# Kernel tuning notes

Hardware: AMD Instinct MI355X
Metric: run time of the kernel (lower is better)

The kernel has to match this reference:

```python
import jax, jax.numpy as jnp
import numpy as np
import math

D_MODEL = 512
NUM_HEADS = 8
HEAD_DIM = D_MODEL // NUM_HEADS
B, L = 2, 2048
LN_EPS = 1e-5
DEN_EPS = 1e-5


def setup_inputs() -> dict:
    key = jax.random.key(0)
    ks = jax.random.split(key, 6)
    s = 1.0 / math.sqrt(D_MODEL)
    return {
        "x": jax.random.normal(ks[0], (B, L, D_MODEL), dtype=jnp.float32),
        "Wqkv": jax.random.normal(ks[1], (D_MODEL, 3 * D_MODEL), dtype=jnp.float32) * s,
        "bqkv": jnp.zeros((3 * D_MODEL,), dtype=jnp.float32),
        "Wout": jax.random.normal(ks[2], (D_MODEL, D_MODEL), dtype=jnp.float32) * s,
        "bout": jnp.zeros((D_MODEL,), dtype=jnp.float32),
        "ln_gamma": jnp.ones((D_MODEL,), dtype=jnp.float32),
        "ln_beta": jnp.zeros((D_MODEL,), dtype=jnp.float32),
        "decay_logits": jnp.full((NUM_HEADS,), 5.0, dtype=jnp.float32),
    }


def reference(x, Wqkv, bqkv, Wout, bout, ln_gamma, ln_beta, decay_logits):
    Bv, Lv, D = x.shape
    H = decay_logits.shape[0]
    E = D // H

    qkv = x @ Wqkv + bqkv                                   # [B,L,3D]
    q, k, v = jnp.split(qkv, 3, axis=-1)
    q = q.reshape(Bv, Lv, H, E)
    k = k.reshape(Bv, Lv, H, E)
    v = v.reshape(Bv, Lv, H, E)

    # ELU feature map + 1 -> positive features; scale q by 1/sqrt(E)
    q = (jax.nn.elu(q) + 1.0) / jnp.sqrt(jnp.asarray(E, x.dtype))
    k = jax.nn.elu(k) + 1.0

    lambdas = jax.nn.sigmoid(decay_logits).reshape(1, 1, H, 1)   # [1,1,H,1]
    t = jnp.arange(Lv, dtype=x.dtype).reshape(1, Lv, 1, 1)       # [1,L,1,1]
    decay_k = jnp.power(lambdas, -t)   # lambda^{-t}
    decay_q = jnp.power(lambdas, t)    # lambda^{t}

    k_dec = k * decay_k                                          # [B,L,H,E]
    kv = jnp.einsum('blhe,blhf->blhef', k_dec, v)                # [B,L,H,E,E]
    memory = jnp.cumsum(kv, axis=1)                              # prefix-sum scan over L
    k_sum = jnp.cumsum(k_dec, axis=1)                            # [B,L,H,E]

    q_dec = q * decay_q
    num = jnp.einsum('blhe,blhef->blhf', q_dec, memory)          # [B,L,H,E]
    den = jnp.einsum('blhe,blhe->blh', q_dec, k_sum)[..., None] + DEN_EPS
    out = (num / den).reshape(Bv, Lv, D)

    out = out @ Wout + bout

    # LayerNorm (eval mode; dropout is identity)
    mu = jnp.mean(out, axis=-1, keepdims=True)
    var = jnp.var(out, axis=-1, keepdims=True)
    out = (out - mu) / jnp.sqrt(var + LN_EPS) * ln_gamma + ln_beta
    return out
```

## Files before the change

kernel.cpp:

```cpp
#include <hip/hip_runtime.h>
#include <math.h>

#define B_ 2
#define L_ 2048
#define D_ 512
#define H_ 8
#define E_ 64
#define CHUNK 32
#define NCH 64
#define DEN_EPS_ 1e-5f
#define LN_EPS_ 1e-5f

typedef __bf16 bf16x8 __attribute__((ext_vector_type(8)));
typedef __bf16 bf16x4 __attribute__((ext_vector_type(4)));
typedef float  f32x4  __attribute__((ext_vector_type(4)));

__device__ __forceinline__ float sigm(float x) { return 1.f / (1.f + expf(-x)); }
__device__ __forceinline__ float elu1(float x) { return x > 0.f ? x + 1.f : expf(x); }

__device__ __forceinline__ void async_cp16(const void* g, void* l) {
    __builtin_amdgcn_global_load_lds(
        (const __attribute__((address_space(1))) void*)g,
        (__attribute__((address_space(3))) void*)l, 16, 0, 0);
}

#define SWZ4(row, q) ((((q) ^ ((row) & 3)) * 8))

__global__ __launch_bounds__(256) void k_prep_w(
    const float* __restrict__ W1, __bf16* __restrict__ D1,
    const float* __restrict__ W2, __bf16* __restrict__ D2)
{
    const int t = threadIdx.x;
    const int bx = blockIdx.x;
    const float* src; __bf16* dst; int N, xt;
    if (bx < 24) { src = W1; dst = D1; N = 1536; xt = bx; }
    else         { src = W2; dst = D2; N = 512;  xt = bx - 24; }
    const int K = 512;

    __shared__ __bf16 tile[64][68];
    const int kb = blockIdx.y * 64, nb = xt * 64;
    const int rr = t >> 4, cc4 = (t & 15) * 4;
#pragma unroll
    for (int p = 0; p < 4; p++) {
        int k = rr + p * 16;
        float4 v = *(const float4*)&src[(size_t)(kb + k) * N + nb + cc4];
        tile[k][cc4 + 0] = (__bf16)v.x;
        tile[k][cc4 + 1] = (__bf16)v.y;
        tile[k][cc4 + 2] = (__bf16)v.z;
        tile[k][cc4 + 3] = (__bf16)v.w;
    }
    __syncthreads();
#pragma unroll
    for (int p = 0; p < 4; p++) {
        int n = rr + p * 16;
        bf16x4 o;
        o[0] = tile[cc4 + 0][n];
        o[1] = tile[cc4 + 1][n];
        o[2] = tile[cc4 + 2][n];
        o[3] = tile[cc4 + 3][n];
        *(bf16x4*)&dst[(size_t)(nb + n) * K + kb + cc4] = o;
    }
}

__global__ __launch_bounds__(256) void k_mfma_qkv_g(
    const float* __restrict__ X, const __bf16* __restrict__ Bt,
    const float* __restrict__ bias, const float* __restrict__ dl,
    __bf16* __restrict__ Qb, __bf16* __restrict__ Kb, __bf16* __restrict__ Vb,
    __bf16* __restrict__ Gt, float* __restrict__ gn)
{
    __shared__ __bf16 lds[28672];
    const int t = threadIdx.x;
    const int w = t >> 6, lane = t & 63;
    const int wm = w >> 1, wn = w & 1;
    const int ll = lane & 15, quad = lane >> 4;
    const int m0 = blockIdx.y * 64, n0 = blockIdx.x * 128;
    const int h0 = n0 >> 6;

    f32x4 acc[3][2][4] = {};
    const int sr = t >> 2;
    const int c4 = t & 3;
    const int skz = ((c4 ^ (sr & 3)) * 8);

    float4 pa0, pa1;
    auto fetchA = [&](int k0) {
        const float* ap = X + (size_t)(m0 + sr) * D_ + k0 + skz;
        pa0 = *(const float4*)ap;
        pa1 = *(const float4*)(ap + 4);
    };
    auto issueB = [&](int k0, int buf) {
        const int bb = buf * 14336 + 2048;
#pragma unroll
        for (int s = 0; s < 3; s++)
#pragma unroll
            for (int half = 0; half < 2; half++)
                async_cp16(&Bt[(size_t)(s * 512 + n0 + half * 64 + sr) * D_ + k0 + skz],
                           &lds[bb + s * 4096 + (half * 64 + w * 16) * 32]);
    };
    auto writeA = [&](int buf) {
        bf16x8 o;
        o[0] = (__bf16)pa0.x; o[1] = (__bf16)pa0.y;
        o[2] = (__bf16)pa0.z; o[3] = (__bf16)pa0.w;
        o[4] = (__bf16)pa1.x; o[5] = (__bf16)pa1.y;
        o[6] = (__bf16)pa1.z; o[7] = (__bf16)pa1.w;
        *(bf16x8*)&lds[buf * 14336 + sr * 32 + c4 * 8] = o;
    };

    fetchA(0);
    issueB(0, 0);
    writeA(0);
    __syncthreads();

    for (int k0 = 0; k0 < D_; k0 += 32) {
        const int buf = (k0 >> 5) & 1, nbuf = buf ^ 1;
        const int nk = k0 + 32;
        if (nk < D_) { fetchA(nk); issueB(nk, nbuf); }
        const int ao = buf * 14336, bo = ao + 2048;
        bf16x8 afr[2];
#pragma unroll
        for (int im = 0; im < 2; im++) {
            int ra = wm * 32 + im * 16 + ll;
            afr[im] = *(const bf16x8*)&lds[ao + ra * 32 + SWZ4(ra, quad)];
        }
#pragma unroll
        for (int s = 0; s < 3; s++) {
            bf16x8 bfr[4];
#pragma unroll
            for (int in = 0; in < 4; in++) {
                int rb = wn * 64 + in * 16 + ll;
                bfr[in] = *(const bf16x8*)&lds[bo + s * 4096 + rb * 32 + SWZ4(rb, quad)];
            }
#pragma unroll
            for (int im = 0; im < 2; im++)
#pragma unroll
                for (int in = 0; in < 4; in++)
                    acc[s][im][in] = __builtin_amdgcn_mfma_f32_16x16x32_bf16(
                        afr[im], bfr[in], acc[s][im][in], 0, 0, 0);
        }
        if (nk < D_) writeA(nbuf);
        __syncthreads();
    }

    const int h = h0 + wn;
    const float lam = sigm(dl[h]);
    const float l2  = log2f(lam);
    __bf16* Kwt = &lds[w * 4096];
    __bf16* Vtw = &lds[w * 4096 + 2048];

    float wk8[2][4];
#pragma unroll
    for (int im = 0; im < 2; im++)
#pragma unroll
        for (int r = 0; r < 4; r++) {
            int i = (im * 16 + quad * 4 + r) & 31;
            wk8[im][r] = exp2f(l2 * (float)(CHUNK - 1 - i));
        }

#pragma unroll
    for (int im = 0; im < 2; im++) {
#pragma unroll
        for (int in = 0; in < 4; in++) {
            int nc = wn * 64 + in * 16 + ll;
            int e  = nc & 63;
            float bq = bias[n0 + nc];
            float bk = bias[512 + n0 + nc];
            float bv = bias[1024 + n0 + nc];
#pragma unroll
            for (int r = 0; r < 4; r++) {
                int mr = wm * 32 + im * 16 + quad * 4 + r;
                int m = m0 + mr, bb2 = m >> 11, l = m & 2047;
                size_t off = ((size_t)((bb2 * H_ + h) * L_ + l)) * E_ + e;
                float vq = elu1(acc[0][im][in][r] + bq) * 0.125f;
                float vk = elu1(acc[1][im][in][r] + bk);
                float vv = acc[2][im][in][r] + bv;
                Qb[off] = (__bf16)vq;
                Kb[off] = (__bf16)vk;
                Vb[off] = (__bf16)vv;
                int i = mr & 31;
                int col = ((i >> 3) ^ (e & 3)) * 8 + (i & 7);
                Kwt[e * 32 + col] = (__bf16)(vk * wk8[im][r]);
                Vtw[e * 32 + col] = (__bf16)vv;
            }
        }
    }

    const int bb2 = m0 >> 11;
    const int bh = bb2 * H_ + h;
    const int nchunk = ((m0 & 2047) >> 5) + wm;

    {
        float ga = 0.f;
#pragma unroll
        for (int ci = 0; ci < 4; ci++) {
            int colb = ((ci ^ (lane & 3)) * 8);
#pragma unroll
            for (int j = 0; j < 8; j++) ga += (float)Kwt[lane * 32 + colb + j];
        }
        gn[((size_t)bh * NCH + nchunk) * E_ + lane] = ga;
    }

    f32x4 gac[4][4] = {};
#pragma unroll
    for (int a = 0; a < 4; a++) {
        int raf = a * 16 + ll;
        bf16x8 av = *(const bf16x8*)&Vtw[raf * 32 + SWZ4(raf, quad)];
#pragma unroll
        for (int b2 = 0; b2 < 4; b2++) {
            int rbe = b2 * 16 + ll;
            bf16x8 kv = *(const bf16x8*)&Kwt[rbe * 32 + SWZ4(rbe, quad)];
            gac[a][b2] = __builtin_amdgcn_mfma_f32_16x16x32_bf16(av, kv, gac[a][b2], 0, 0, 0);
        }
    }
    size_t gbase = ((size_t)bh * NCH + nchunk) * 4096;
#pragma unroll
    for (int a = 0; a < 4; a++)
#pragma unroll
        for (int b2 = 0; b2 < 4; b2++)
#pragma unroll
            for (int r = 0; r < 4; r++) {
                int f = a * 16 + quad * 4 + r;
                int e = b2 * 16 + ll;
                Gt[gbase + (size_t)f * 64 + e] = (__bf16)gac[a][b2][r];
            }
}

__global__ __launch_bounds__(64) void k_scan_par(
    const __bf16* __restrict__ Gt, const float* __restrict__ gn,
    const float* __restrict__ dl,
    __bf16* __restrict__ Sb, float* __restrict__ zl)
{
    const int lane = threadIdx.x;
    const int bh = blockIdx.x >> 6;
    const int j  = blockIdx.x & 63;
    const float lam = sigm(dl[bh & 7]);
    const float dC  = exp2f(32.f * log2f(lam));

    const size_t base = ((size_t)bh * NCH) * 4096 + (size_t)j * 64 + lane;

    __bf16 g[NCH];
#pragma unroll
    for (int n = 0; n < NCH; n++) g[n] = Gt[base + (size_t)n * 4096];

    float s = 0.f;
#pragma unroll
    for (int n = 0; n < NCH; n++) {
        Sb[base + (size_t)n * 4096] = (__bf16)(lam * s);
        s = fmaf(dC, s, (float)g[n]);
    }

    float gv = gn[((size_t)bh * NCH + lane) * E_ + j];
    float wf = dC;
#pragma unroll
    for (int k = 1; k < 64; k <<= 1) {
        float up = __shfl_up(gv, k);
        if (lane >= k) gv = fmaf(wf, up, gv);
        wf = wf * wf;
    }
    float zex = __shfl_up(gv, 1);
    if (lane == 0) zex = 0.f;
    zl[((size_t)bh * NCH + lane) * E_ + j] = lam * zex;
}

__global__ __launch_bounds__(256) void k_attn(
    const __bf16* __restrict__ Qb, const __bf16* __restrict__ Kb,
    const __bf16* __restrict__ Vb,
    const __bf16* __restrict__ Sb, const float* __restrict__ zl,
    const float* __restrict__ dl, __bf16* __restrict__ Out)
{
    __shared__ __bf16 Qw[32][64];
    __shared__ __bf16 Kw[32][64];
    __shared__ __bf16 Vt[64][40];
    __shared__ __bf16 A1[32][40];
    __shared__ float  den[32];
    __shared__ float  zz[64];

    const int t  = threadIdx.x;
    const int bx = blockIdx.x;
    const int n = bx & 63, h = (bx >> 6) & 7, bb = bx >> 9;
    const int bh = bb * H_ + h;
    const float lam = sigm(dl[h]);
    const float l2  = log2f(lam);

    const int w = t >> 6, lane = t & 63;
    const int ll = lane & 15, quad = lane >> 4;
    const int fw = w * 16;
    const size_t sbase = ((size_t)bh * NCH + n) * 4096;

    bf16x8 bS0 = *(const bf16x8*)&Sb[sbase + (size_t)(fw + ll) * 64 + quad * 8];
    bf16x8 bS1 = *(const bf16x8*)&Sb[sbase + (size_t)(fw + ll) * 64 + 32 + quad * 8];

    {
        int i = t >> 3, e0c = t & 7;
        size_t src = ((size_t)bh * L_ + n * CHUNK + i) * E_ + e0c * 8;
        float wq = exp2f(l2 * (float)i);
        float wk = exp2f(-l2 * (float)i);
        bf16x8 q8 = *(const bf16x8*)&Qb[src];
        bf16x8 k8 = *(const bf16x8*)&Kb[src];
        bf16x8 v8 = *(const bf16x8*)&Vb[src];
        bf16x8 qo, ko;
        int e0 = e0c * 8;
#pragma unroll
        for (int q = 0; q < 8; q++) {
            qo[q] = (__bf16)((float)q8[q] * wq);
            ko[q] = (__bf16)((float)k8[q] * wk);
            Vt[e0 + q][i] = v8[q];
        }
        int cs = (e0c ^ (i & 7)) * 8;
        *(bf16x8*)&Qw[i][cs] = qo;
        *(bf16x8*)&Kw[i][cs] = ko;
        if (t < 64) zz[t] = zl[((size_t)bh * NCH + n) * E_ + t];
    }
    __syncthreads();

    {
        const int wm = w >> 1, wn = w & 1;
        int ra = wm * 16 + ll, rb = wn * 16 + ll;
        f32x4 accA = {};
#pragma unroll
        for (int ks = 0; ks < 2; ks++) {
            bf16x8 a = *(const bf16x8*)&Qw[ra][((ks * 4 + quad) ^ (ra & 7)) * 8];
            bf16x8 b = *(const bf16x8*)&Kw[rb][((ks * 4 + quad) ^ (rb & 7)) * 8];
            accA = __builtin_amdgcn_mfma_f32_16x16x32_bf16(a, b, accA, 0, 0, 0);
        }
        int j = wn * 16 + ll;
#pragma unroll
        for (int r = 0; r < 4; r++) {
            int i = wm * 16 + quad * 4 + r;
            A1[i][j] = (__bf16)(j <= i ? accA[r] : 0.f);
        }
    }
    __syncthreads();

    if (t < 32) {
        float rs = 0.f;
#pragma unroll
        for (int k8 = 0; k8 < 4; k8++) {
            bf16x8 aa = *(const bf16x8*)&A1[t][k8 * 8];
#pragma unroll
            for (int q = 0; q < 8; q++) rs += (float)aa[q];
        }
        float qz = 0.f;
#pragma unroll
        for (int e8 = 0; e8 < 8; e8++) {
            bf16x8 qq = *(const bf16x8*)&Qw[t][(e8 ^ (t & 7)) * 8];
#pragma unroll
            for (int q = 0; q < 8; q++) qz += (float)qq[q] * zz[e8 * 8 + q];
        }
        den[t] = rs + qz + DEN_EPS_;
    }

    f32x4 acc1[2] = {}, acc2[2] = {};
    {
        bf16x8 bV = *(const bf16x8*)&Vt[fw + ll][quad * 8];
#pragma unroll
        for (int im = 0; im < 2; im++) {
            bf16x8 aA = *(const bf16x8*)&A1[im * 16 + ll][quad * 8];
            acc1[im] = __builtin_amdgcn_mfma_f32_16x16x32_bf16(aA, bV, acc1[im], 0, 0, 0);
        }
#pragma unroll
        for (int im = 0; im < 2; im++) {
            int ra = im * 16 + ll;
            bf16x8 aQ0 = *(const bf16x8*)&Qw[ra][((quad) ^ (ra & 7)) * 8];
            bf16x8 aQ1 = *(const bf16x8*)&Qw[ra][((4 + quad) ^ (ra & 7)) * 8];
            acc2[im] = __builtin_amdgcn_mfma_f32_16x16x32_bf16(aQ0, bS0, acc2[im], 0, 0, 0);
            acc2[im] = __builtin_amdgcn_mfma_f32_16x16x32_bf16(aQ1, bS1, acc2[im], 0, 0, 0);
        }
    }
    __syncthreads();

#pragma unroll
    for (int im = 0; im < 2; im++)
#pragma unroll
        for (int r = 0; r < 4; r++) {
            int i = im * 16 + quad * 4 + r;
            float o = (acc1[im][r] + acc2[im][r]) / den[i];
            Out[((size_t)bb * L_ + n * CHUNK + i) * D_ + h * E_ + fw + ll] = (__bf16)o;
        }
}

__global__ __launch_bounds__(256) void k_mfma_out_ln(
    const __bf16* __restrict__ Ab, const __bf16* __restrict__ Bt,
    const float* __restrict__ bias, const float* __restrict__ gam,
    const float* __restrict__ bet, float* __restrict__ Y)
{
    __shared__ __bf16 lds[33792];
    __shared__ float gaml[512], betl[512], bl[512];
    __shared__ float redS[4][16], redQ[4][16];
    __shared__ float mv[16][2];

    const int t = threadIdx.x;
    const int w = t >> 6, lane = t & 63;
    const int ll = lane & 15, quad = lane >> 4;
    const int m0 = blockIdx.x * 16;

    {
        float2 g = *(const float2*)&gam[t * 2];
        float2 b2 = *(const float2*)&bet[t * 2];
        float2 bo = *(const float2*)&bias[t * 2];
        gaml[t * 2] = g.x;  gaml[t * 2 + 1] = g.y;
        betl[t * 2] = b2.x; betl[t * 2 + 1] = b2.y;
        bl[t * 2]   = bo.x; bl[t * 2 + 1]   = bo.y;
    }

    f32x4 acc[8] = {};
    const int sr  = t >> 2;
    const int skz = (((t & 3) ^ (sr & 3)) * 8);

    auto issue = [&](int k0, int buf) {
        if (t < 64)
            async_cp16(&Ab[(size_t)(m0 + sr) * D_ + k0 + skz], &lds[buf * 512]);
#pragma unroll
        for (int p = 0; p < 8; p++)
            async_cp16(&Bt[(size_t)(p * 64 + sr) * D_ + k0 + skz],
                       &lds[1024 + buf * 16384 + (p * 64 + w * 16) * 32]);
    };

    issue(0, 0);
    __syncthreads();

    for (int k0 = 0; k0 < D_; k0 += 32) {
        const int buf = (k0 >> 5) & 1, nbuf = buf ^ 1;
        const int nk = k0 + 32;
        if (nk < D_) issue(nk, nbuf);
        const int ao = buf * 512, bo = 1024 + buf * 16384;
        bf16x8 a = *(const bf16x8*)&lds[ao + ll * 32 + SWZ4(ll, quad)];
#pragma unroll
        for (int in = 0; in < 8; in++) {
            int rb = w * 128 + in * 16 + ll;
            bf16x8 b = *(const bf16x8*)&lds[bo + rb * 32 + SWZ4(rb, quad)];
            acc[in] = __builtin_amdgcn_mfma_f32_16x16x32_bf16(a, b, acc[in], 0, 0, 0);
        }
        __syncthreads();
    }

    float vals[8][4];
    float ps[4] = {}, pq[4] = {};
#pragma unroll
    for (int in = 0; in < 8; in++) {
        int col = w * 128 + in * 16 + ll;
        float bv = bl[col];
#pragma unroll
        for (int r = 0; r < 4; r++) {
            float v = acc[in][r] + bv;
            vals[in][r] = v;
            ps[r] += v;
            pq[r] += v * v;
        }
    }
#pragma unroll
    for (int r = 0; r < 4; r++) {
        float s = ps[r], q = pq[r];
        s += __shfl_xor(s, 1); q += __shfl_xor(q, 1);
        s += __shfl_xor(s, 2); q += __shfl_xor(q, 2);
        s += __shfl_xor(s, 4); q += __shfl_xor(q, 4);
        s += __shfl_xor(s, 8); q += __shfl_xor(q, 8);
        if (ll == 0) {
            int row = quad * 4 + r;
            redS[w][row] = s;
            redQ[w][row] = q;
        }
    }
    __syncthreads();
    if (t < 16) {
        float S = redS[0][t] + redS[1][t] + redS[2][t] + redS[3][t];
        float Q = redQ[0][t] + redQ[1][t] + redQ[2][t] + redQ[3][t];
        float mu  = S * (1.f / 512.f);
        float var = Q * (1.f / 512.f) - mu * mu;
        mv[t][0] = mu;
        mv[t][1] = rsqrtf(var + LN_EPS_);
    }
    __syncthreads();
#pragma unroll
    for (int r = 0; r < 4; r++) {
        int row = quad * 4 + r;
        float mu = mv[row][0], rs = mv[row][1];
#pragma unroll
        for (int in = 0; in < 8; in++) {
            int col = w * 128 + in * 16 + ll;
            Y[(size_t)(m0 + row) * D_ + col] =
                (vals[in][r] - mu) * rs * gaml[col] + betl[col];
        }
    }
}

extern "C" void kernel_launch(void* const* d_in, const int* in_sizes, int n_in,
                              void* d_out, int out_size, void* d_ws, size_t ws_size,
                              hipStream_t stream)
{
    const float* x    = (const float*)d_in[0];
    const float* Wqkv = (const float*)d_in[1];
    const float* bqkv = (const float*)d_in[2];
    const float* Wout = (const float*)d_in[3];
    const float* bout = (const float*)d_in[4];
    const float* gam  = (const float*)d_in[5];
    const float* bet  = (const float*)d_in[6];
    const float* dl   = (const float*)d_in[7];
    float* out = (float*)d_out;

    const size_t NBHLE = (size_t)B_ * H_ * L_ * E_;
    const size_t NG    = (size_t)B_ * H_ * NCH * E_ * E_;
    const size_t Ng    = (size_t)B_ * H_ * NCH * E_;

    char* p = (char*)d_ws;
    __bf16* Gt  = (__bf16*)p;    p += NG * 2;
    __bf16* Sb  = (__bf16*)p;    p += NG * 2;
    float*  gn  = (float*)p;     p += Ng * 4;
    float*  zl  = (float*)p;     p += Ng * 4;
    __bf16* Qb  = (__bf16*)p;    p += NBHLE * 2;
    __bf16* Kb  = (__bf16*)p;    p += NBHLE * 2;
    __bf16* Vb  = (__bf16*)p;    p += NBHLE * 2;
    __bf16* WqkvT = (__bf16*)p;  p += (size_t)1536 * 512 * 2;
    __bf16* WoutT = (__bf16*)p;  p += (size_t)512 * 512 * 2;
    __bf16* Ao    = (__bf16*)p;  p += NBHLE * 2;

    dim3 blk(256);
    k_prep_w      <<<dim3(32, 8), blk, 0, stream>>>(Wqkv, WqkvT, Wout, WoutT);
    k_mfma_qkv_g  <<<dim3(4, 64), blk, 0, stream>>>(x, WqkvT, bqkv, dl,
                                                    Qb, Kb, Vb, Gt, gn);
    k_scan_par    <<<dim3(1024),  dim3(64), 0, stream>>>(Gt, gn, dl, Sb, zl);
    k_attn        <<<dim3(1024),  blk, 0, stream>>>(Qb, Kb, Vb, Sb, zl, dl, Ao);
    k_mfma_out_ln <<<dim3(256),   blk, 0, stream>>>(Ao, WoutT, bout, gam, bet, out);
}
```

Baseline: 128.6 us.

## Fuse all stages into one persistent kernel with grid-wide atomic barriers

Replaces the five separate kernel launches with a single persistent kernel of 256 blocks. The stages (weight transpose, QKV GEMM, scan, chunked attention, output GEMM with LayerNorm) are separated by software grid barriers built on atomic counters, and each stage reuses one shared-memory buffer. This is meant to remove launch overhead and inter-kernel gaps. In exchange, stages that used 1024 blocks now loop inside 256 blocks, the output GEMM loses its double buffering, and correctness depends on all 256 blocks being co-resident.

```diff
diff --git a/kernel.cpp b/kernel.cpp
--- a/kernel.cpp
+++ b/kernel.cpp
@@ -10,6 +10,7 @@
 #define NCH 64
 #define DEN_EPS_ 1e-5f
 #define LN_EPS_ 1e-5f
+#define NBLK 256
 
 typedef __bf16 bf16x8 __attribute__((ext_vector_type(8)));
 typedef __bf16 bf16x4 __attribute__((ext_vector_type(4)));
@@ -26,458 +27,460 @@
 
 #define SWZ4(row, q) ((((q) ^ ((row) & 3)) * 8))
 
-__global__ __launch_bounds__(256) void k_prep_w(
-    const float* __restrict__ W1, __bf16* __restrict__ D1,
-    const float* __restrict__ W2, __bf16* __restrict__ D2)
-{
-    const int t = threadIdx.x;
-    const int bx = blockIdx.x;
-    const float* src; __bf16* dst; int N, xt;
-    if (bx < 24) { src = W1; dst = D1; N = 1536; xt = bx; }
-    else         { src = W2; dst = D2; N = 512;  xt = bx - 24; }
-    const int K = 512;
-
-    __shared__ __bf16 tile[64][68];
-    const int kb = blockIdx.y * 64, nb = xt * 64;
-    const int rr = t >> 4, cc4 = (t & 15) * 4;
-#pragma unroll
-    for (int p = 0; p < 4; p++) {
-        int k = rr + p * 16;
-        float4 v = *(const float4*)&src[(size_t)(kb + k) * N + nb + cc4];
-        tile[k][cc4 + 0] = (__bf16)v.x;
-        tile[k][cc4 + 1] = (__bf16)v.y;
-        tile[k][cc4 + 2] = (__bf16)v.z;
-        tile[k][cc4 + 3] = (__bf16)v.w;
+__device__ __forceinline__ void gbar(unsigned int* bar, int idx) {
+    __syncthreads();
+    if (threadIdx.x == 0) {
+        __threadfence();
+        atomicAdd(&bar[idx], 1u);
+        while (__hip_atomic_load(&bar[idx], __ATOMIC_RELAXED,
+                                 __HIP_MEMORY_SCOPE_AGENT) < (unsigned)NBLK)
+            __builtin_amdgcn_s_sleep(8);
+        __threadfence();
     }
     __syncthreads();
-#pragma unroll
-    for (int p = 0; p < 4; p++) {
-        int n = rr + p * 16;
-        bf16x4 o;
-        o[0] = tile[cc4 + 0][n];
-        o[1] = tile[cc4 + 1][n];
-        o[2] = tile[cc4 + 2][n];
-        o[3] = tile[cc4 + 3][n];
-        *(bf16x4*)&dst[(size_t)(nb + n) * K + kb + cc4] = o;
-    }
 }
 
-__global__ __launch_bounds__(256) void k_mfma_qkv_g(
-    const float* __restrict__ X, const __bf16* __restrict__ Bt,
-    const float* __restrict__ bias, const float* __restrict__ dl,
+struct AttnS {
+    __bf16 Qw[32][64];
+    __bf16 Kw[32][64];
+    __bf16 Vt[64][40];
+    __bf16 A1[32][40];
+    float  den[32];
+    float  zz[64];
+};
+struct OutS {
+    __bf16 lds[16896];
+    float  gaml[512], betl[512], bl[512];
+    float  redS[4][16], redQ[4][16];
+    float  mv[16][2];
+};
+
+__global__ __launch_bounds__(256) void k_mega(
+    const float* __restrict__ X,  const float* __restrict__ W1,
+    const float* __restrict__ W2, const float* __restrict__ bqkv,
+    const float* __restrict__ bout, const float* __restrict__ gam,
+    const float* __restrict__ bet,  const float* __restrict__ dl,
+    __bf16* __restrict__ WqkvT, __bf16* __restrict__ WoutT,
     __bf16* __restrict__ Qb, __bf16* __restrict__ Kb, __bf16* __restrict__ Vb,
-    __bf16* __restrict__ Gt, float* __restrict__ gn)
+    __bf16* __restrict__ Gt, float* __restrict__ gn,
+    __bf16* __restrict__ Sb, float* __restrict__ zl,
+    __bf16* __restrict__ Ao, float* __restrict__ out,
+    unsigned int* bar)
 {
-    __shared__ __bf16 lds[28672];
-    const int t = threadIdx.x;
-    const int w = t >> 6, lane = t & 63;
-    const int wm = w >> 1, wn = w & 1;
-    const int ll = lane & 15, quad = lane >> 4;
-    const int m0 = blockIdx.y * 64, n0 = blockIdx.x * 128;
-    const int h0 = n0 >> 6;
-
-    f32x4 acc[3][2][4] = {};
-    const int sr = t >> 2;
-    const int c4 = t & 3;
-    const int skz = ((c4 ^ (sr & 3)) * 8);
-
-    float4 pa0, pa1;
-    auto fetchA = [&](int k0) {
-        const float* ap = X + (size_t)(m0 + sr) * D_ + k0 + skz;
-        pa0 = *(const float4*)ap;
-        pa1 = *(const float4*)(ap + 4);
-    };
-    auto issueB = [&](int k0, int buf) {
-        const int bb = buf * 14336 + 2048;
-#pragma unroll
-        for (int s = 0; s < 3; s++)
-#pragma unroll
-            for (int half = 0; half < 2; half++)
-                async_cp16(&Bt[(size_t)(s * 512 + n0 + half * 64 + sr) * D_ + k0 + skz],
-                           &lds[bb + s * 4096 + (half * 64 + w * 16) * 32]);
-    };
-    auto writeA = [&](int buf) {
-        bf16x8 o;
-        o[0] = (__bf16)pa0.x; o[1] = (__bf16)pa0.y;
-        o[2] = (__bf16)pa0.z; o[3] = (__bf16)pa0.w;
-        o[4] = (__bf16)pa1.x; o[5] = (__bf16)pa1.y;
-        o[6] = (__bf16)pa1.z; o[7] = (__bf16)pa1.w;
-        *(bf16x8*)&lds[buf * 14336 + sr * 32 + c4 * 8] = o;
-    };
-
-    fetchA(0);
-    issueB(0, 0);
-    writeA(0);
-    __syncthreads();
-
-    for (int k0 = 0; k0 < D_; k0 += 32) {
-        const int buf = (k0 >> 5) & 1, nbuf = buf ^ 1;
-        const int nk = k0 + 32;
-        if (nk < D_) { fetchA(nk); issueB(nk, nbuf); }
-        const int ao = buf * 14336, bo = ao + 2048;
-        bf16x8 afr[2];
-#pragma unroll
-        for (int im = 0; im < 2; im++) {
-            int ra = wm * 32 + im * 16 + ll;
-            afr[im] = *(const bf16x8*)&lds[ao + ra * 32 + SWZ4(ra, quad)];
-        }
-#pragma unroll
-        for (int s = 0; s < 3; s++) {
-            bf16x8 bfr[4];
-#pragma unroll
-            for (int in = 0; in < 4; in++) {
-                int rb = wn * 64 + in * 16 + ll;
-                bfr[in] = *(const bf16x8*)&lds[bo + s * 4096 + rb * 32 + SWZ4(rb, quad)];
-            }
-#pragma unroll
-            for (int im = 0; im < 2; im++)
-#pragma unroll
-                for (int in = 0; in < 4; in++)
-                    acc[s][im][in] = __builtin_amdgcn_mfma_f32_16x16x32_bf16(
-                        afr[im], bfr[in], acc[s][im][in], 0, 0, 0);
-        }
-        if (nk < D_) writeA(nbuf);
-        __syncthreads();
-    }
-
-    const int h = h0 + wn;
-    const float lam = sigm(dl[h]);
-    const float l2  = log2f(lam);
-    __bf16* Kwt = &lds[w * 4096];
-    __bf16* Vtw = &lds[w * 4096 + 2048];
-
-    float wk8[2][4];
-#pragma unroll
-    for (int im = 0; im < 2; im++)
-#pragma unroll
-        for (int r = 0; r < 4; r++) {
-            int i = (im * 16 + quad * 4 + r) & 31;
-            wk8[im][r] = exp2f(l2 * (float)(CHUNK - 1 - i));
-        }
-
-#pragma unroll
-    for (int im = 0; im < 2; im++) {
-#pragma unroll
-        for (int in = 0; in < 4; in++) {
-            int nc = wn * 64 + in * 16 + ll;
-            int e  = nc & 63;
-            float bq = bias[n0 + nc];
-            float bk = bias[512 + n0 + nc];
-            float bv = bias[1024 + n0 + nc];
-#pragma unroll
-            for (int r = 0; r < 4; r++) {
-                int mr = wm * 32 + im * 16 + quad * 4 + r;
-                int m = m0 + mr, bb2 = m >> 11, l = m & 2047;
-                size_t off = ((size_t)((bb2 * H_ + h) * L_ + l)) * E_ + e;
-                float vq = elu1(acc[0][im][in][r] + bq) * 0.125f;
-                float vk = elu1(acc[1][im][in][r] + bk);
-                float vv = acc[2][im][in][r] + bv;
-                Qb[off] = (__bf16)vq;
-                Kb[off] = (__bf16)vk;
-                Vb[off] = (__bf16)vv;
-                int i = mr & 31;
-                int col = ((i >> 3) ^ (e & 3)) * 8 + (i & 7);
-                Kwt[e * 32 + col] = (__bf16)(vk * wk8[im][r]);
-                Vtw[e * 32 + col] = (__bf16)vv;
-            }
-        }
-    }
-
-    const int bb2 = m0 >> 11;
-    const int bh = bb2 * H_ + h;
-    const int nchunk = ((m0 & 2047) >> 5) + wm;
-
-    {
-        float ga = 0.f;
-#pragma unroll
-        for (int ci = 0; ci < 4; ci++) {
-            int colb = ((ci ^ (lane & 3)) * 8);
-#pragma unroll
-            for (int j = 0; j < 8; j++) ga += (float)Kwt[lane * 32 + colb + j];
-        }
-        gn[((size_t)bh * NCH + nchunk) * E_ + lane] = ga;
-    }
-
-    f32x4 gac[4][4] = {};
-#pragma unroll
-    for (int a = 0; a < 4; a++) {
-        int raf = a * 16 + ll;
-        bf16x8 av = *(const bf16x8*)&Vtw[raf * 32 + SWZ4(raf, quad)];
-#pragma unroll
-        for (int b2 = 0; b2 < 4; b2++) {
-            int rbe = b2 * 16 + ll;
-            bf16x8 kv = *(const bf16x8*)&Kwt[rbe * 32 + SWZ4(rbe, quad)];
-            gac[a][b2] = __builtin_amdgcn_mfma_f32_16x16x32_bf16(av, kv, gac[a][b2], 0, 0, 0);
-        }
-    }
-    size_t gbase = ((size_t)bh * NCH + nchunk) * 4096;
-#pragma unroll
-    for (int a = 0; a < 4; a++)
-#pragma unroll
-        for (int b2 = 0; b2 < 4; b2++)
-#pragma unroll
-            for (int r = 0; r < 4; r++) {
-                int f = a * 16 + quad * 4 + r;
-                int e = b2 * 16 + ll;
-                Gt[gbase + (size_t)f * 64 + e] = (__bf16)gac[a][b2][r];
-            }
-}
-
-__global__ __launch_bounds__(64) void k_scan_par(
-    const __bf16* __restrict__ Gt, const float* __restrict__ gn,
-    const float* __restrict__ dl,
-    __bf16* __restrict__ Sb, float* __restrict__ zl)
-{
-    const int lane = threadIdx.x;
-    const int bh = blockIdx.x >> 6;
-    const int j  = blockIdx.x & 63;
-    const float lam = sigm(dl[bh & 7]);
-    const float dC  = exp2f(32.f * log2f(lam));
-
-    const size_t base = ((size_t)bh * NCH) * 4096 + (size_t)j * 64 + lane;
-
-    __bf16 g[NCH];
-#pragma unroll
-    for (int n = 0; n < NCH; n++) g[n] = Gt[base + (size_t)n * 4096];
-
-    float s = 0.f;
-#pragma unroll
-    for (int n = 0; n < NCH; n++) {
-        Sb[base + (size_t)n * 4096] = (__bf16)(lam * s);
-        s = fmaf(dC, s, (float)g[n]);
-    }
-
-    float gv = gn[((size_t)bh * NCH + lane) * E_ + j];
-    float wf = dC;
-#pragma unroll
-    for (int k = 1; k < 64; k <<= 1) {
-        float up = __shfl_up(gv, k);
-        if (lane >= k) gv = fmaf(wf, up, gv);
-        wf = wf * wf;
-    }
-    float zex = __shfl_up(gv, 1);
-    if (lane == 0) zex = 0.f;
-    zl[((size_t)bh * NCH + lane) * E_ + j] = lam * zex;
-}
-
-__global__ __launch_bounds__(256) void k_attn(
-    const __bf16* __restrict__ Qb, const __bf16* __restrict__ Kb,
-    const __bf16* __restrict__ Vb,
-    const __bf16* __restrict__ Sb, const float* __restrict__ zl,
-    const float* __restrict__ dl, __bf16* __restrict__ Out)
-{
-    __shared__ __bf16 Qw[32][64];
-    __shared__ __bf16 Kw[32][64];
-    __shared__ __bf16 Vt[64][40];
-    __shared__ __bf16 A1[32][40];
-    __shared__ float  den[32];
-    __shared__ float  zz[64];
-
+    __shared__ __align__(16) char smem[57344];
     const int t  = threadIdx.x;
-    const int bx = blockIdx.x;
-    const int n = bx & 63, h = (bx >> 6) & 7, bb = bx >> 9;
-    const int bh = bb * H_ + h;
-    const float lam = sigm(dl[h]);
-    const float l2  = log2f(lam);
-
+    const int vb = blockIdx.x;
     const int w = t >> 6, lane = t & 63;
     const int ll = lane & 15, quad = lane >> 4;
-    const int fw = w * 16;
-    const size_t sbase = ((size_t)bh * NCH + n) * 4096;
-
-    bf16x8 bS0 = *(const bf16x8*)&Sb[sbase + (size_t)(fw + ll) * 64 + quad * 8];
-    bf16x8 bS1 = *(const bf16x8*)&Sb[sbase + (size_t)(fw + ll) * 64 + 32 + quad * 8];
 
     {
-        int i = t >> 3, e0c = t & 7;
-        size_t src = ((size_t)bh * L_ + n * CHUNK + i) * E_ + e0c * 8;
-        float wq = exp2f(l2 * (float)i);
-        float wk = exp2f(-l2 * (float)i);
-        bf16x8 q8 = *(const bf16x8*)&Qb[src];
-        bf16x8 k8 = *(const bf16x8*)&Kb[src];
-        bf16x8 v8 = *(const bf16x8*)&Vb[src];
-        bf16x8 qo, ko;
-        int e0 = e0c * 8;
-#pragma unroll
-        for (int q = 0; q < 8; q++) {
-            qo[q] = (__bf16)((float)q8[q] * wq);
-            ko[q] = (__bf16)((float)k8[q] * wk);
-            Vt[e0 + q][i] = v8[q];
-        }
-        int cs = (e0c ^ (i & 7)) * 8;
-        *(bf16x8*)&Qw[i][cs] = qo;
-        *(bf16x8*)&Kw[i][cs] = ko;
-        if (t < 64) zz[t] = zl[((size_t)bh * NCH + n) * E_ + t];
+        __bf16 (*tile)[68] = (__bf16(*)[68])smem;
+        const int xt_ = vb & 31, ky = vb >> 5;
+        const float* src; __bf16* dst; int N, xt;
+        if (xt_ < 24) { src = W1; dst = WqkvT; N = 1536; xt = xt_; }
+        else          { src = W2; dst = WoutT; N = 512;  xt = xt_ - 24; }
+        const int K = 512;
+        const int kb = ky * 64, nb = xt * 64;
+        const int rr = t >> 4, cc4 = (t & 15) * 4;
+#pragma unroll
+        for (int p = 0; p < 4; p++) {
+            int k = rr + p * 16;
+            float4 v = *(const float4*)&src[(size_t)(kb + k) * N + nb + cc4];
+            tile[k][cc4 + 0] = (__bf16)v.x;
+            tile[k][cc4 + 1] = (__bf16)v.y;
+            tile[k][cc4 + 2] = (__bf16)v.z;
+            tile[k][cc4 + 3] = (__bf16)v.w;
+        }
+        __syncthreads();
+#pragma unroll
+        for (int p = 0; p < 4; p++) {
+            int n = rr + p * 16;
+            bf16x4 o;
+            o[0] = tile[cc4 + 0][n];
+            o[1] = tile[cc4 + 1][n];
+            o[2] = tile[cc4 + 2][n];
+            o[3] = tile[cc4 + 3][n];
+            *(bf16x4*)&dst[(size_t)(nb + n) * K + kb + cc4] = o;
+        }
     }
-    __syncthreads();
+    gbar(bar, 0);
 
     {
+        __bf16* lds = (__bf16*)smem;
         const int wm = w >> 1, wn = w & 1;
-        int ra = wm * 16 + ll, rb = wn * 16 + ll;
-        f32x4 accA = {};
-#pragma unroll
-        for (int ks = 0; ks < 2; ks++) {
-            bf16x8 a = *(const bf16x8*)&Qw[ra][((ks * 4 + quad) ^ (ra & 7)) * 8];
-            bf16x8 b = *(const bf16x8*)&Kw[rb][((ks * 4 + quad) ^ (rb & 7)) * 8];
-            accA = __builtin_amdgcn_mfma_f32_16x16x32_bf16(a, b, accA, 0, 0, 0);
-        }
-        int j = wn * 16 + ll;
-#pragma unroll
-        for (int r = 0; r < 4; r++) {
-            int i = wm * 16 + quad * 4 + r;
-            A1[i][j] = (__bf16)(j <= i ? accA[r] : 0.f);
-        }
+        const int m0 = (vb >> 2) * 64, n0 = (vb & 3) * 128;
+        const int h0 = n0 >> 6;
+
+        f32x4 acc[3][2][4] = {};
+        const int sr = t >> 2;
+        const int c4 = t & 3;
+        const int skz = ((c4 ^ (sr & 3)) * 8);
+
+        float4 pa0, pa1;
+        auto fetchA = [&](int k0) {
+            const float* ap = X + (size_t)(m0 + sr) * D_ + k0 + skz;
+            pa0 = *(const float4*)ap;
+            pa1 = *(const float4*)(ap + 4);
+        };
+        auto issueB = [&](int k0, int buf) {
+            const int bb = buf * 14336 + 2048;
+#pragma unroll
+            for (int s = 0; s < 3; s++)
+#pragma unroll
+                for (int half = 0; half < 2; half++)
+                    async_cp16(&WqkvT[(size_t)(s * 512 + n0 + half * 64 + sr) * D_ + k0 + skz],
+                               &lds[bb + s * 4096 + (half * 64 + w * 16) * 32]);
+        };
+        auto writeA = [&](int buf) {
+            bf16x8 o;
+            o[0] = (__bf16)pa0.x; o[1] = (__bf16)pa0.y;
+            o[2] = (__bf16)pa0.z; o[3] = (__bf16)pa0.w;
+            o[4] = (__bf16)pa1.x; o[5] = (__bf16)pa1.y;
+            o[6] = (__bf16)pa1.z; o[7] = (__bf16)pa1.w;
+            *(bf16x8*)&lds[buf * 14336 + sr * 32 + c4 * 8] = o;
+        };
+
+        fetchA(0);
+        issueB(0, 0);
+        writeA(0);
+        __syncthreads();
+
+        for (int k0 = 0; k0 < D_; k0 += 32) {
+            const int buf = (k0 >> 5) & 1, nbuf = buf ^ 1;
+            const int nk = k0 + 32;
+            if (nk < D_) { fetchA(nk); issueB(nk, nbuf); }
+            const int ao = buf * 14336, bo = ao + 2048;
+            bf16x8 afr[2];
+#pragma unroll
+            for (int im = 0; im < 2; im++) {
+                int ra = wm * 32 + im * 16 + ll;
+                afr[im] = *(const bf16x8*)&lds[ao + ra * 32 + SWZ4(ra, quad)];
+            }
+#pragma unroll
+            for (int s = 0; s < 3; s++) {
+                bf16x8 bfr[4];
+#pragma unroll
+                for (int in = 0; in < 4; in++) {
+                    int rb = wn * 64 + in * 16 + ll;
+                    bfr[in] = *(const bf16x8*)&lds[bo + s * 4096 + rb * 32 + SWZ4(rb, quad)];
+                }
+#pragma unroll
+                for (int im = 0; im < 2; im++)
+#pragma unroll
+                    for (int in = 0; in < 4; in++)
+                        acc[s][im][in] = __builtin_amdgcn_mfma_f32_16x16x32_bf16(
+                            afr[im], bfr[in], acc[s][im][in], 0, 0, 0);
+            }
+            if (nk < D_) writeA(nbuf);
+            __syncthreads();
+        }
+
+        const int h = h0 + wn;
+        const float lam = sigm(dl[h]);
+        const float l2  = log2f(lam);
+        __bf16* Kwt = &lds[w * 4096];
+        __bf16* Vtw = &lds[w * 4096 + 2048];
+
+        float wk8[2][4];
+#pragma unroll
+        for (int im = 0; im < 2; im++)
+#pragma unroll
+            for (int r = 0; r < 4; r++) {
+                int i = (im * 16 + quad * 4 + r) & 31;
+                wk8[im][r] = exp2f(l2 * (float)(CHUNK - 1 - i));
+            }
+
+#pragma unroll
+        for (int im = 0; im < 2; im++) {
+#pragma unroll
+            for (int in = 0; in < 4; in++) {
+                int nc = wn * 64 + in * 16 + ll;
+                int e  = nc & 63;
+                float bq = bqkv[n0 + nc];
+                float bk = bqkv[512 + n0 + nc];
+                float bv = bqkv[1024 + n0 + nc];
+#pragma unroll
+                for (int r = 0; r < 4; r++) {
+                    int mr = wm * 32 + im * 16 + quad * 4 + r;
+                    int m = m0 + mr, bb2 = m >> 11, l = m & 2047;
+                    size_t off = ((size_t)((bb2 * H_ + h) * L_ + l)) * E_ + e;
+                    float vq = elu1(acc[0][im][in][r] + bq) * 0.125f;
+                    float vk = elu1(acc[1][im][in][r] + bk);
+                    float vv = acc[2][im][in][r] + bv;
+                    Qb[off] = (__bf16)vq;
+                    Kb[off] = (__bf16)vk;
+                    Vb[off] = (__bf16)vv;
+                    int i = mr & 31;
+                    int col = ((i >> 3) ^ (e & 3)) * 8 + (i & 7);
+                    Kwt[e * 32 + col] = (__bf16)(vk * wk8[im][r]);
+                    Vtw[e * 32 + col] = (__bf16)vv;
+                }
+            }
+        }
+
+        const int bb2 = m0 >> 11;
+        const int bh = bb2 * H_ + h;
+        const int nchunk = ((m0 & 2047) >> 5) + wm;
+
+        {
+            float ga = 0.f;
+#pragma unroll
+            for (int ci = 0; ci < 4; ci++) {
+                int colb = ((ci ^ (lane & 3)) * 8);
+#pragma unroll
+                for (int j = 0; j < 8; j++) ga += (float)Kwt[lane * 32 + colb + j];
+            }
+            gn[((size_t)bh * NCH + nchunk) * E_ + lane] = ga;
+        }
+
+        f32x4 gac[4][4] = {};
+#pragma unroll
+        for (int a = 0; a < 4; a++) {
+            int raf = a * 16 + ll;
+            bf16x8 av = *(const bf16x8*)&Vtw[raf * 32 + SWZ4(raf, quad)];
+#pragma unroll
+            for (int b2 = 0; b2 < 4; b2++) {
+                int rbe = b2 * 16 + ll;
+                bf16x8 kv = *(const bf16x8*)&Kwt[rbe * 32 + SWZ4(rbe, quad)];
+                gac[a][b2] = __builtin_amdgcn_mfma_f32_16x16x32_bf16(av, kv, gac[a][b2], 0, 0, 0);
+            }
+        }
+        size_t gbase = ((size_t)bh * NCH + nchunk) * 4096;
+#pragma unroll
+        for (int a = 0; a < 4; a++)
+#pragma unroll
+            for (int b2 = 0; b2 < 4; b2++)
+#pragma unroll
+                for (int r = 0; r < 4; r++) {
+                    int f = a * 16 + quad * 4 + r;
+                    int e = b2 * 16 + ll;
+                    Gt[gbase + (size_t)f * 64 + e] = (__bf16)gac[a][b2][r];
+                }
     }
-    __syncthreads();
-
-    if (t < 32) {
-        float rs = 0.f;
-#pragma unroll
-        for (int k8 = 0; k8 < 4; k8++) {
-            bf16x8 aa = *(const bf16x8*)&A1[t][k8 * 8];
-#pragma unroll
-            for (int q = 0; q < 8; q++) rs += (float)aa[q];
-        }
-        float qz = 0.f;
-#pragma unroll
-        for (int e8 = 0; e8 < 8; e8++) {
-            bf16x8 qq = *(const bf16x8*)&Qw[t][(e8 ^ (t & 7)) * 8];
-#pragma unroll
-            for (int q = 0; q < 8; q++) qz += (float)qq[q] * zz[e8 * 8 + q];
-        }
-        den[t] = rs + qz + DEN_EPS_;
+    gbar(bar, 1);
+
+    {
+        const int unit = vb * 4 + w;
+        const int bh = unit >> 6;
+        const int j  = unit & 63;
+        const float lam = sigm(dl[bh & 7]);
+        const float dC  = exp2f(32.f * log2f(lam));
+
+        const size_t base = ((size_t)bh * NCH) * 4096 + (size_t)j * 64 + lane;
+
+        __bf16 g[NCH];
+#pragma unroll
+        for (int n = 0; n < NCH; n++) g[n] = Gt[base + (size_t)n * 4096];
+
+        float s = 0.f;
+#pragma unroll
+        for (int n = 0; n < NCH; n++) {
+            Sb[base + (size_t)n * 4096] = (__bf16)(lam * s);
+            s = fmaf(dC, s, (float)g[n]);
+        }
+
+        float gv = gn[((size_t)bh * NCH + lane) * E_ + j];
+        float wf = dC;
+#pragma unroll
+        for (int k = 1; k < 64; k <<= 1) {
+            float up = __shfl_up(gv, k);
+            if (lane >= k) gv = fmaf(wf, up, gv);
+            wf = wf * wf;
+        }
+        float zex = __shfl_up(gv, 1);
+        if (lane == 0) zex = 0.f;
+        zl[((size_t)bh * NCH + lane) * E_ + j] = lam * zex;
     }
-
-    f32x4 acc1[2] = {}, acc2[2] = {};
+    gbar(bar, 2);
+
     {
-        bf16x8 bV = *(const bf16x8*)&Vt[fw + ll][quad * 8];
-#pragma unroll
-        for (int im = 0; im < 2; im++) {
-            bf16x8 aA = *(const bf16x8*)&A1[im * 16 + ll][quad * 8];
-            acc1[im] = __builtin_amdgcn_mfma_f32_16x16x32_bf16(aA, bV, acc1[im], 0, 0, 0);
-        }
-#pragma unroll
-        for (int im = 0; im < 2; im++) {
-            int ra = im * 16 + ll;
-            bf16x8 aQ0 = *(const bf16x8*)&Qw[ra][((quad) ^ (ra & 7)) * 8];
-            bf16x8 aQ1 = *(const bf16x8*)&Qw[ra][((4 + quad) ^ (ra & 7)) * 8];
-            acc2[im] = __builtin_amdgcn_mfma_f32_16x16x32_bf16(aQ0, bS0, acc2[im], 0, 0, 0);
-            acc2[im] = __builtin_amdgcn_mfma_f32_16x16x32_bf16(aQ1, bS1, acc2[im], 0, 0, 0);
+        AttnS& S = *(AttnS*)smem;
+        for (int u = 0; u < 4; u++) {
+            const int bx = vb * 4 + u;
+            const int n = bx & 63, h = (bx >> 6) & 7, bb = bx >> 9;
+            const int bh = bb * H_ + h;
+            const float lam = sigm(dl[h]);
+            const float l2  = log2f(lam);
+            const int fw = w * 16;
+            const size_t sbase = ((size_t)bh * NCH + n) * 4096;
+
+            bf16x8 bS0 = *(const bf16x8*)&Sb[sbase + (size_t)(fw + ll) * 64 + quad * 8];
+            bf16x8 bS1 = *(const bf16x8*)&Sb[sbase + (size_t)(fw + ll) * 64 + 32 + quad * 8];
+
+            {
+                int i = t >> 3, e0c = t & 7;
+                size_t src = ((size_t)bh * L_ + n * CHUNK + i) * E_ + e0c * 8;
+                float wq = exp2f(l2 * (float)i);
+                float wk = exp2f(-l2 * (float)i);
+                bf16x8 q8 = *(const bf16x8*)&Qb[src];
+                bf16x8 k8 = *(const bf16x8*)&Kb[src];
+                bf16x8 v8 = *(const bf16x8*)&Vb[src];
+                bf16x8 qo, ko;
+                int e0 = e0c * 8;
+#pragma unroll
+                for (int q = 0; q < 8; q++) {
+                    qo[q] = (__bf16)((float)q8[q] * wq);
+                    ko[q] = (__bf16)((float)k8[q] * wk);
+                    S.Vt[e0 + q][i] = v8[q];
+                }
+                int cs = (e0c ^ (i & 7)) * 8;
+                *(bf16x8*)&S.Qw[i][cs] = qo;
+                *(bf16x8*)&S.Kw[i][cs] = ko;
+                if (t < 64) S.zz[t] = zl[((size_t)bh * NCH + n) * E_ + t];
+            }
+            __syncthreads();
+
+            {
+                const int wm = w >> 1, wn = w & 1;
+                int ra = wm * 16 + ll, rb = wn * 16 + ll;
+                f32x4 accA = {};
+#pragma unroll
+                for (int ks = 0; ks < 2; ks++) {
+                    bf16x8 a = *(const bf16x8*)&S.Qw[ra][((ks * 4 + quad) ^ (ra & 7)) * 8];
+                    bf16x8 b = *(const bf16x8*)&S.Kw[rb][((ks * 4 + quad) ^ (rb & 7)) * 8];
+                    accA = __builtin_amdgcn_mfma_f32_16x16x32_bf16(a, b, accA, 0, 0, 0);
+                }
+                int j = wn * 16 + ll;
+#pragma unroll
+                for (int r = 0; r < 4; r++) {
+                    int i = wm * 16 + quad * 4 + r;
+                    S.A1[i][j] = (__bf16)(j <= i ? accA[r] : 0.f);
+                }
+            }
+            __syncthreads();
+
+            if (t < 32) {
+                float rs = 0.f;
+#pragma unroll
+                for (int k8 = 0; k8 < 4; k8++) {
+                    bf16x8 aa = *(const bf16x8*)&S.A1[t][k8 * 8];
+#pragma unroll
+                    for (int q = 0; q < 8; q++) rs += (float)aa[q];
+                }
+                float qz = 0.f;
+#pragma unroll
+                for (int e8 = 0; e8 < 8; e8++) {
+                    bf16x8 qq = *(const bf16x8*)&S.Qw[t][(e8 ^ (t & 7)) * 8];
+#pragma unroll
+                    for (int q = 0; q < 8; q++) qz += (float)qq[q] * S.zz[e8 * 8 + q];
+                }
+                S.den[t] = rs + qz + DEN_EPS_;
+            }
+
+            f32x4 acc1[2] = {}, acc2[2] = {};
+            {
+                bf16x8 bV = *(const bf16x8*)&S.Vt[fw + ll][quad * 8];
+#pragma unroll
+                for (int im = 0; im < 2; im++) {
+                    bf16x8 aA = *(const bf16x8*)&S.A1[im * 16 + ll][quad * 8];
+                    acc1[im] = __builtin_amdgcn_mfma_f32_16x16x32_bf16(aA, bV, acc1[im], 0, 0, 0);
+                }
+#pragma unroll
+                for (int im = 0; im < 2; im++) {
+                    int ra = im * 16 + ll;
+                    bf16x8 aQ0 = *(const bf16x8*)&S.Qw[ra][((quad) ^ (ra & 7)) * 8];
+                    bf16x8 aQ1 = *(const bf16x8*)&S.Qw[ra][((4 + quad) ^ (ra & 7)) * 8];
+                    acc2[im] = __builtin_amdgcn_mfma_f32_16x16x32_bf16(aQ0, bS0, acc2[im], 0, 0, 0);
+                    acc2[im] = __builtin_amdgcn_mfma_f32_16x16x32_bf16(aQ1, bS1, acc2[im], 0, 0, 0);
+                }
+            }
+            __syncthreads();
+
+#pragma unroll
+            for (int im = 0; im < 2; im++)
+#pragma unroll
+                for (int r = 0; r < 4; r++) {
+                    int i = im * 16 + quad * 4 + r;
+                    float o = (acc1[im][r] + acc2[im][r]) / S.den[i];
+                    Ao[((size_t)bb * L_ + n * CHUNK + i) * D_ + h * E_ + fw + ll] = (__bf16)o;
+                }
+            __syncthreads();
         }
     }
-    __syncthreads();
-
-#pragma unroll
-    for (int im = 0; im < 2; im++)
-#pragma unroll
-        for (int r = 0; r < 4; r++) {
-            int i = im * 16 + quad * 4 + r;
-            float o = (acc1[im][r] + acc2[im][r]) / den[i];
-            Out[((size_t)bb * L_ + n * CHUNK + i) * D_ + h * E_ + fw + ll] = (__bf16)o;
-        }
-}
-
-__global__ __launch_bounds__(256) void k_mfma_out_ln(
-    const __bf16* __restrict__ Ab, const __bf16* __restrict__ Bt,
-    const float* __restrict__ bias, const float* __restrict__ gam,
-    const float* __restrict__ bet, float* __restrict__ Y)
-{
-    __shared__ __bf16 lds[33792];
-    __shared__ float gaml[512], betl[512], bl[512];
-    __shared__ float redS[4][16], redQ[4][16];
-    __shared__ float mv[16][2];
-
-    const int t = threadIdx.x;
-    const int w = t >> 6, lane = t & 63;
-    const int ll = lane & 15, quad = lane >> 4;
-    const int m0 = blockIdx.x * 16;
+    gbar(bar, 3);
 
     {
-        float2 g = *(const float2*)&gam[t * 2];
-        float2 b2 = *(const float2*)&bet[t * 2];
-        float2 bo = *(const float2*)&bias[t * 2];
-        gaml[t * 2] = g.x;  gaml[t * 2 + 1] = g.y;
-        betl[t * 2] = b2.x; betl[t * 2 + 1] = b2.y;
-        bl[t * 2]   = bo.x; bl[t * 2 + 1]   = bo.y;
-    }
-
-    f32x4 acc[8] = {};
-    const int sr  = t >> 2;
-    const int skz = (((t & 3) ^ (sr & 3)) * 8);
-
-    auto issue = [&](int k0, int buf) {
-        if (t < 64)
-            async_cp16(&Ab[(size_t)(m0 + sr) * D_ + k0 + skz], &lds[buf * 512]);
-#pragma unroll
-        for (int p = 0; p < 8; p++)
-            async_cp16(&Bt[(size_t)(p * 64 + sr) * D_ + k0 + skz],
-                       &lds[1024 + buf * 16384 + (p * 64 + w * 16) * 32]);
-    };
-
-    issue(0, 0);
-    __syncthreads();
-
-    for (int k0 = 0; k0 < D_; k0 += 32) {
-        const int buf = (k0 >> 5) & 1, nbuf = buf ^ 1;
-        const int nk = k0 + 32;
-        if (nk < D_) issue(nk, nbuf);
-        const int ao = buf * 512, bo = 1024 + buf * 16384;
-        bf16x8 a = *(const bf16x8*)&lds[ao + ll * 32 + SWZ4(ll, quad)];
-#pragma unroll
-        for (int in = 0; in < 8; in++) {
-            int rb = w * 128 + in * 16 + ll;
-            bf16x8 b = *(const bf16x8*)&lds[bo + rb * 32 + SWZ4(rb, quad)];
-            acc[in] = __builtin_amdgcn_mfma_f32_16x16x32_bf16(a, b, acc[in], 0, 0, 0);
-        }
-        __syncthreads();
-    }
-
-    float vals[8][4];
-    float ps[4] = {}, pq[4] = {};
-#pragma unroll
-    for (int in = 0; in < 8; in++) {
-        int col = w * 128 + in * 16 + ll;
-        float bv = bl[col];
-#pragma unroll
-        for (int r = 0; r < 4; r++) {
-            float v = acc[in][r] + bv;
-            vals[in][r] = v;
-            ps[r] += v;
-            pq[r] += v * v;
-        }
-    }
-#pragma unroll
-    for (int r = 0; r < 4; r++) {
-        float s = ps[r], q = pq[r];
-        s += __shfl_xor(s, 1); q += __shfl_xor(q, 1);
-        s += __shfl_xor(s, 2); q += __shfl_xor(q, 2);
-        s += __shfl_xor(s, 4); q += __shfl_xor(q, 4);
-        s += __shfl_xor(s, 8); q += __shfl_xor(q, 8);
-        if (ll == 0) {
-            int row = quad * 4 + r;
-            redS[w][row] = s;
-            redQ[w][row] = q;
-        }
-    }
-    __syncthreads();
-    if (t < 16) {
-        float S = redS[0][t] + redS[1][t] + redS[2][t] + redS[3][t];
-        float Q = redQ[0][t] + redQ[1][t] + redQ[2][t] + redQ[3][t];
-        float mu  = S * (1.f / 512.f);
-        float var = Q * (1.f / 512.f) - mu * mu;
-        mv[t][0] = mu;
-        mv[t][1] = rsqrtf(var + LN_EPS_);
-    }
-    __syncthreads();
-#pragma unroll
-    for (int r = 0; r < 4; r++) {
-        int row = quad * 4 + r;
-        float mu = mv[row][0], rs = mv[row][1];
+        OutS& S = *(OutS*)smem;
+        const int m0 = vb * 16;
+
+        {
+            float2 g = *(const float2*)&gam[t * 2];
+            float2 b2 = *(const float2*)&bet[t * 2];
+            float2 bo = *(const float2*)&bout[t * 2];
+            S.gaml[t * 2] = g.x;  S.gaml[t * 2 + 1] = g.y;
+            S.betl[t * 2] = b2.x; S.betl[t * 2 + 1] = b2.y;
+            S.bl[t * 2]   = bo.x; S.bl[t * 2 + 1]   = bo.y;
+        }
+
+        f32x4 acc[8] = {};
+        const int sr  = t >> 2;
+        const int skz = (((t & 3) ^ (sr & 3)) * 8);
+
+        for (int k0 = 0; k0 < D_; k0 += 32) {
+            if (t < 64)
+                async_cp16(&Ao[(size_t)(m0 + sr) * D_ + k0 + skz], &S.lds[0]);
+#pragma unroll
+            for (int p = 0; p < 8; p++)
+                async_cp16(&WoutT[(size_t)(p * 64 + sr) * D_ + k0 + skz],
+                           &S.lds[512 + (p * 64 + w * 16) * 32]);
+            __syncthreads();
+            bf16x8 a = *(const bf16x8*)&S.lds[ll * 32 + SWZ4(ll, quad)];
+#pragma unroll
+            for (int in = 0; in < 8; in++) {
+                int rb = w * 128 + in * 16 + ll;
+                bf16x8 b = *(const bf16x8*)&S.lds[512 + rb * 32 + SWZ4(rb, quad)];
+                acc[in] = __builtin_amdgcn_mfma_f32_16x16x32_bf16(a, b, acc[in], 0, 0, 0);
+            }
+            __syncthreads();
+        }
+
+        float vals[8][4];
+        float ps[4] = {}, pq[4] = {};
 #pragma unroll
         for (int in = 0; in < 8; in++) {
             int col = w * 128 + in * 16 + ll;
-            Y[(size_t)(m0 + row) * D_ + col] =
-                (vals[in][r] - mu) * rs * gaml[col] + betl[col];
+            float bv = S.bl[col];
+#pragma unroll
+            for (int r = 0; r < 4; r++) {
+                float v = acc[in][r] + bv;
+                vals[in][r] = v;
+                ps[r] += v;
+                pq[r] += v * v;
+            }
+        }
+#pragma unroll
+        for (int r = 0; r < 4; r++) {
+            float s = ps[r], q = pq[r];
+            s += __shfl_xor(s, 1); q += __shfl_xor(q, 1);
+            s += __shfl_xor(s, 2); q += __shfl_xor(q, 2);
+            s += __shfl_xor(s, 4); q += __shfl_xor(q, 4);
+            s += __shfl_xor(s, 8); q += __shfl_xor(q, 8);
+            if (ll == 0) {
+                int row = quad * 4 + r;
+                S.redS[w][row] = s;
+                S.redQ[w][row] = q;
+            }
+        }
+        __syncthreads();
+        if (t < 16) {
+            float Su = S.redS[0][t] + S.redS[1][t] + S.redS[2][t] + S.redS[3][t];
+            float Qu = S.redQ[0][t] + S.redQ[1][t] + S.redQ[2][t] + S.redQ[3][t];
+            float mu  = Su * (1.f / 512.f);
+            float var = Qu * (1.f / 512.f) - mu * mu;
+            S.mv[t][0] = mu;
+            S.mv[t][1] = rsqrtf(var + LN_EPS_);
+        }
+        __syncthreads();
+#pragma unroll
+        for (int r = 0; r < 4; r++) {
+            int row = quad * 4 + r;
+            float mu = S.mv[row][0], rs = S.mv[row][1];
+#pragma unroll
+            for (int in = 0; in < 8; in++) {
+                int col = w * 128 + in * 16 + ll;
+                out[(size_t)(m0 + row) * D_ + col] =
+                    (vals[in][r] - mu) * rs * S.gaml[col] + S.betl[col];
+            }
         }
     }
 }
@@ -501,6 +504,7 @@
     const size_t Ng    = (size_t)B_ * H_ * NCH * E_;
 
     char* p = (char*)d_ws;
+    unsigned int* bar = (unsigned int*)p;  p += 256;
     __bf16* Gt  = (__bf16*)p;    p += NG * 2;
     __bf16* Sb  = (__bf16*)p;    p += NG * 2;
     float*  gn  = (float*)p;     p += Ng * 4;
@@ -512,11 +516,8 @@
     __bf16* WoutT = (__bf16*)p;  p += (size_t)512 * 512 * 2;
     __bf16* Ao    = (__bf16*)p;  p += NBHLE * 2;
 
-    dim3 blk(256);
-    k_prep_w      <<<dim3(32, 8), blk, 0, stream>>>(Wqkv, WqkvT, Wout, WoutT);
-    k_mfma_qkv_g  <<<dim3(4, 64), blk, 0, stream>>>(x, WqkvT, bqkv, dl,
-                                                    Qb, Kb, Vb, Gt, gn);
-    k_scan_par    <<<dim3(1024),  dim3(64), 0, stream>>>(Gt, gn, dl, Sb, zl);
-    k_attn        <<<dim3(1024),  blk, 0, stream>>>(Qb, Kb, Vb, Sb, zl, dl, Ao);
-    k_mfma_out_ln <<<dim3(256),   blk, 0, stream>>>(Ao, WoutT, bout, gam, bet, out);
+    hipMemsetAsync(bar, 0, 4 * sizeof(unsigned int), stream);
+    k_mega<<<dim3(NBLK), dim3(256), 0, stream>>>(
+        x, Wqkv, Wout, bqkv, bout, gam, bet, dl,
+        WqkvT, WoutT, Qb, Kb, Vb, Gt, gn, Sb, zl, Ao, out, bar);
 }
```

Measured after the change: 223.5 us. +73.7%, slower.
